# Optimization experiments

Measured on AMD Instinct MI355X. Metric: run time of the kernel, lower is better.

The kernel has to match this reference:

```python
import jax, jax.numpy as jnp
import numpy as np

N = 50000      # num nodes
IN = 256       # in_channels
H = 4          # heads
C = 64         # out_channels per head (concat=False -> out_dim = C)
HOPS = 3       # max_hops == num hops provided
E = 400000     # edges per hop
NEG_SLOPE = 0.2


def setup_inputs() -> dict:
    key = jax.random.key(0)
    ks = jax.random.split(key, 10)
    s_in = 1.0 / np.sqrt(IN)
    s_c = 1.0 / np.sqrt(C)
    return {
        "x": jax.random.normal(ks[0], (N, IN), jnp.float32),
        "ei0": jax.random.randint(ks[1], (2, E), 0, N, dtype=jnp.int32),
        "ei1": jax.random.randint(ks[2], (2, E), 0, N, dtype=jnp.int32),
        "ei2": jax.random.randint(ks[3], (2, E), 0, N, dtype=jnp.int32),
        # shared left/right projections (lin_l / lin_r, shared across hops)
        "W_l": jax.random.normal(ks[4], (IN, H * C), jnp.float32) * s_in,
        "b_l": jnp.zeros((H * C,), jnp.float32),
        "W_r": jax.random.normal(ks[5], (IN, H * C), jnp.float32) * s_in,
        "b_r": jnp.zeros((H * C,), jnp.float32),
        # hop-specific attention vectors and output biases
        "att": jax.random.normal(ks[6], (HOPS, H, C), jnp.float32) * s_c,
        "bias": jnp.zeros((HOPS, C), jnp.float32),
        # hop gate (single Linear since gate_hidden=None)
        "W_gate": jax.random.normal(ks[7], (IN, HOPS), jnp.float32) * s_in,
        "b_gate": jnp.zeros((HOPS,), jnp.float32),
    }


def _segment_softmax(logits, seg, n):
    # logits: [E, H], seg: [E] destination node ids
    m = jax.ops.segment_max(logits, seg, num_segments=n)          # [N, H]
    m = jnp.where(jnp.isfinite(m), m, 0.0)                        # empty segments -> 0
    ex = jnp.exp(logits - m[seg])
    s = jax.ops.segment_sum(ex, seg, num_segments=n)              # [N, H]
    return ex / (s[seg] + 1e-16)


def _gatv2_hop(x_l, x_r, edge_index, att_k, bias_k):
    # x_l, x_r: [N, H, C] shared projections; edge_index: [2, Ek]
    src, dst = edge_index[0], edge_index[1]
    s = jax.nn.leaky_relu(x_l[src] + x_r[dst], NEG_SLOPE)         # [Ek, H, C]
    alpha = jnp.einsum("ehc,hc->eh", s, att_k)                    # [Ek, H]
    alpha = _segment_softmax(alpha, dst, N)
    msg = jax.ops.segment_sum(x_l[src] * alpha[..., None], dst, num_segments=N)  # [N, H, C]
    return msg.mean(axis=1) + bias_k                              # concat=False -> head mean, [N, C]


def reference(x, ei0, ei1, ei2, W_l, b_l, W_r, b_r, att, bias, W_gate, b_gate):
    # shared projections computed once
    x_l = (x @ W_l + b_l).reshape(N, H, C)
    x_r = (x @ W_r + b_r).reshape(N, H, C)

    # hop 0 gets self-loops (add_self_loops=True); higher hops do not
    ar = jnp.arange(N, dtype=ei0.dtype)
    ei0_sl = jnp.concatenate([ei0, jnp.stack([ar, ar])], axis=1)
    edges = [ei0_sl, ei1, ei2]

    messages = jnp.stack(
        [_gatv2_hop(x_l, x_r, edges[k], att[k], bias[k]) for k in range(HOPS)],
        axis=1,
    )  # [N, HOPS, C]

    logits = x @ W_gate + b_gate                                  # [N, HOPS]
    weights = jax.nn.softmax(logits, axis=-1)
    out = jnp.einsum("nkc,nk->nc", messages, weights)             # [N, C]
    return out
```

## Files before the change

### kernel.cpp

```cpp
#include <hip/hip_runtime.h>
#include <math.h>

#define N_NODES 50000
#define IN_DIM 256
#define HEADS 4
#define CDIM 64
#define HC 256
#define HOPS 3
#define EDGES 400000
#define NEG_SLOPE 0.2f
#define SEG (EDGES + N_NODES)
#define TOT_E (3 * EDGES + N_NODES)
#define CAP 40

#define NB_GATE  ((N_NODES + 3) / 4)
#define NB_PACKW ((IN_DIM * 2 * HC) / 256)
#define NB_SCAT  ((TOT_E + 255) / 256)
#define GB 64
#define GEMM_BLOCKS ((N_NODES + GB - 1) / GB)
#define AP 264
#define BP 40

typedef unsigned short ushort;
using short8  = __attribute__((ext_vector_type(8))) short;
using floatx4 = __attribute__((ext_vector_type(4))) float;
using f32x2   = __attribute__((ext_vector_type(2))) float;

__device__ __forceinline__ void decode_flat(int f, int& k, int& e)
{
    if (f < SEG)              { k = 0; e = f; }
    else if (f < SEG + EDGES) { k = 1; e = f - SEG; }
    else                      { k = 2; e = f - SEG - EDGES; }
}

__device__ __forceinline__ ushort f2bf(float f)
{
    unsigned u = __float_as_uint(f);
    unsigned r = u + 0x7fffu + ((u >> 16) & 1u);
    return (ushort)(r >> 16);
}

__device__ __forceinline__ f32x2 bf2x(unsigned u)
{
    f32x2 r;
    r.x = __uint_as_float(u << 16);
    r.y = __uint_as_float(u & 0xffff0000u);
    return r;
}

__device__ __forceinline__ f32x2 lrelu2(f32x2 v)
{
    return __builtin_elementwise_max(v, 0.2f * v);
}

__global__ __launch_bounds__(256) void prep(
    const float* __restrict__ X, const float* __restrict__ Wg,
    const float* __restrict__ bg, float* __restrict__ gw,
    ushort* __restrict__ Xb,
    const float* __restrict__ Wl, const float* __restrict__ Wr,
    ushort* __restrict__ WT,
    const int* __restrict__ ei0, const int* __restrict__ ei1,
    const int* __restrict__ ei2, int* __restrict__ cnt,
    int* __restrict__ bucket)
{
    const int blk = blockIdx.x;
    const int tid = threadIdx.x;

    if (blk < NB_GATE) {
        const int node = (blk * 256 + tid) >> 6;
        const int lane = tid & 63;
        if (node >= N_NODES) return;

        float4 xv = ((const float4*)(X + (size_t)node * IN_DIM))[lane];

        union { ushort s[4]; uint2 u; } o;
        o.s[0] = f2bf(xv.x); o.s[1] = f2bf(xv.y);
        o.s[2] = f2bf(xv.z); o.s[3] = f2bf(xv.w);
        ((uint2*)(Xb + (size_t)node * IN_DIM))[lane] = o.u;

        float a0 = 0.f, a1 = 0.f, a2 = 0.f;
        const int i0 = lane * 4;
        a0 += xv.x * Wg[(i0 + 0) * HOPS + 0]; a1 += xv.x * Wg[(i0 + 0) * HOPS + 1]; a2 += xv.x * Wg[(i0 + 0) * HOPS + 2];
        a0 += xv.y * Wg[(i0 + 1) * HOPS + 0]; a1 += xv.y * Wg[(i0 + 1) * HOPS + 1]; a2 += xv.y * Wg[(i0 + 1) * HOPS + 2];
        a0 += xv.z * Wg[(i0 + 2) * HOPS + 0]; a1 += xv.z * Wg[(i0 + 2) * HOPS + 1]; a2 += xv.z * Wg[(i0 + 2) * HOPS + 2];
        a0 += xv.w * Wg[(i0 + 3) * HOPS + 0]; a1 += xv.w * Wg[(i0 + 3) * HOPS + 1]; a2 += xv.w * Wg[(i0 + 3) * HOPS + 2];

        #pragma unroll
        for (int off = 32; off >= 1; off >>= 1) {
            a0 += __shfl_xor(a0, off);
            a1 += __shfl_xor(a1, off);
            a2 += __shfl_xor(a2, off);
        }
        if (lane == 0) {
            float l0 = a0 + bg[0], l1 = a1 + bg[1], l2 = a2 + bg[2];
            float m = fmaxf(l0, fmaxf(l1, l2));
            float e0 = expf(l0 - m), e1 = expf(l1 - m), e2 = expf(l2 - m);
            float inv = 1.f / (e0 + e1 + e2);
            gw[node * HOPS + 0] = e0 * inv;
            gw[node * HOPS + 1] = e1 * inv;
            gw[node * HOPS + 2] = e2 * inv;
        }
    } else if (blk < NB_GATE + NB_PACKW) {
        int id = (blk - NB_GATE) * 256 + tid;
        int n = id >> 8;
        int k = id & 255;
        float v = (n < HC) ? Wl[k * HC + n] : Wr[k * HC + (n - HC)];
        WT[(size_t)n * IN_DIM + k] = f2bf(v);
    } else {
        int f = (blk - NB_GATE - NB_PACKW) * 256 + tid;
        if (f >= TOT_E) return;
        int k, e; decode_flat(f, k, e);
        int s, d;
        if (k == 0 && e >= EDGES) { s = d = e - EDGES; }
        else {
            const int* ei = (k == 0) ? ei0 : (k == 1) ? ei1 : ei2;
            s = ei[e]; d = ei[EDGES + e];
        }
        int pos = atomicAdd(&cnt[k * N_NODES + d], 1);
        if (pos < CAP)
            bucket[((size_t)k * N_NODES + d) * CAP + pos] = s;
    }
}

__global__ __launch_bounds__(256, 2) void gemm_mfma(
    const ushort* __restrict__ Xb, const ushort* __restrict__ WT,
    const float* __restrict__ b_l, const float* __restrict__ b_r,
    ushort* __restrict__ xlb, ushort* __restrict__ xrb, int M)
{
    __shared__ ushort As[GB][AP];
    __shared__ ushort Bs[512][BP];
    const int tid  = threadIdx.x;
    const int wave = tid >> 6, lane = tid & 63;
    const int row0 = blockIdx.x * GB;
    const int wx   = wave * 128;
    const int lrow = lane & 15, lk = (lane >> 4) * 8;

    #pragma unroll
    for (int j = 0; j < 8; j++) {
        int id = tid + 256 * j;
        int r  = id >> 5;
        int c  = (id & 31) * 8;
        int gr = row0 + r;
        uint4 v = make_uint4(0u, 0u, 0u, 0u);
        if (gr < M)
            v = *(const uint4*)(Xb + (size_t)gr * IN_DIM + c);
        *(uint4*)&As[r][c] = v;
    }

    floatx4 acc[4][8];
    #pragma unroll
    for (int i = 0; i < 4; i++)
        #pragma unroll
        for (int j = 0; j < 8; j++)
            acc[i][j] = (floatx4){0.f, 0.f, 0.f, 0.f};

    for (int k0 = 0; k0 < IN_DIM; k0 += 32) {
        __syncthreads();
        #pragma unroll
        for (int j = 0; j < 8; j++) {
            int id = tid + 256 * j;
            int r  = id >> 2;
            int c  = (id & 3) * 8;
            *(uint4*)&Bs[r][c] =
                *(const uint4*)(WT + (size_t)r * IN_DIM + k0 + c);
        }
        __syncthreads();

        short8 af[4], bf[8];
        #pragma unroll
        for (int mi = 0; mi < 4; mi++)
            af[mi] = *(const short8*)&As[mi * 16 + lrow][k0 + lk];
        #pragma unroll
        for (int ni = 0; ni < 8; ni++)
            bf[ni] = *(const short8*)&Bs[wx + ni * 16 + lrow][lk];

        #pragma unroll
        for (int mi = 0; mi < 4; mi++)
            #pragma unroll
            for (int ni = 0; ni < 8; ni++)
                acc[mi][ni] = __builtin_amdgcn_mfma_f32_16x16x32_bf16(
                    bf[ni], af[mi], acc[mi][ni], 0, 0, 0);
    }

    const int csub = (lane >> 4) * 4;
    const bool left = (wx < HC);
    const float*  bvec = left ? b_l : b_r;
    ushort*       obuf = left ? xlb : xrb;
    const int     cbase = left ? wx : wx - HC;
    #pragma unroll
    for (int mi = 0; mi < 4; mi++) {
        int grow = row0 + mi * 16 + lrow;
        if (grow < M) {
            #pragma unroll
            for (int ni = 0; ni < 8; ni++) {
                int lc = cbase + ni * 16 + csub;
                floatx4 v = acc[mi][ni];
                const float4 b = *(const float4*)(bvec + lc);
                union { ushort s[4]; uint2 u; } o;
                o.s[0] = f2bf(v[0] + b.x);
                o.s[1] = f2bf(v[1] + b.y);
                o.s[2] = f2bf(v[2] + b.z);
                o.s[3] = f2bf(v[3] + b.w);
                *(uint2*)(obuf + (size_t)grow * HC + lc) = o.u;
            }
        }
    }
}

__global__ __launch_bounds__(192) void node_all(
    const ushort* __restrict__ xlb, const ushort* __restrict__ xrb,
    const int* __restrict__ cnt, const int* __restrict__ bucket,
    const float* __restrict__ att, const float* __restrict__ gw,
    const float* __restrict__ bias, float* __restrict__ out)
{
    __shared__ float lds[HOPS][CDIM];
    const int n    = blockIdx.x;
    const int k    = threadIdx.x >> 6;
    const int lane = threadIdx.x & 63;
    const int half = lane >> 5;
    const int sub  = lane & 31;
    const unsigned laneoff = (unsigned)sub * 8;

    const int deg = min(cnt[k * N_NODES + n], CAP);
    const int* bk = bucket + ((size_t)k * N_NODES + n) * CAP;

    uint4 rq = *(const uint4*)(xrb + (size_t)n * HC + laneoff);
    f32x2 rr[4] = { bf2x(rq.x), bf2x(rq.y), bf2x(rq.z), bf2x(rq.w) };

    const float4 a0 = ((const float4*)(att + (size_t)k * HC))[sub * 2 + 0];
    const float4 a1 = ((const float4*)(att + (size_t)k * HC))[sub * 2 + 1];
    f32x2 w2[4] = { {a0.x, a0.y}, {a0.z, a0.w}, {a1.x, a1.y}, {a1.z, a1.w} };

    float denom = 0.f;
    f32x2 acc2[4] = { {0.f,0.f}, {0.f,0.f}, {0.f,0.f}, {0.f,0.f} };

    if (deg > 0) {
        const int degm1 = deg - 1;
        int myS = (lane < deg) ? bk[lane] : 0;
        const int npair = (deg + 1) >> 1;

        int s0 = __shfl(myS, min(half, degm1));
        uint4 q = *(const uint4*)(xlb + (unsigned)s0 * HC + laneoff);

        for (int j = 0; j < npair; j++) {
            int sn = __shfl(myS, min(2 * (j + 1) + half, degm1));
            uint4 qn = *(const uint4*)(xlb + (unsigned)sn * HC + laneoff);

            f32x2 f0 = bf2x(q.x), f1 = bf2x(q.y);
            f32x2 f2 = bf2x(q.z), f3 = bf2x(q.w);

            f32x2 pp = w2[0] * lrelu2(f0 + rr[0]);
            pp = __builtin_elementwise_fma(w2[1], lrelu2(f1 + rr[1]), pp);
            pp = __builtin_elementwise_fma(w2[2], lrelu2(f2 + rr[2]), pp);
            pp = __builtin_elementwise_fma(w2[3], lrelu2(f3 + rr[3]), pp);
            float p = pp.x + pp.y;

            p += __shfl_xor(p, 1);
            p += __shfl_xor(p, 2);
            p += __shfl_xor(p, 4);

            bool valid = (2 * j + half) < deg;
            float ex = valid ? __expf(p) : 0.f;
            denom += ex;
            f32x2 ex2 = { ex, ex };
            acc2[0] = __builtin_elementwise_fma(ex2, f0, acc2[0]);
            acc2[1] = __builtin_elementwise_fma(ex2, f1, acc2[1]);
            acc2[2] = __builtin_elementwise_fma(ex2, f2, acc2[2]);
            acc2[3] = __builtin_elementwise_fma(ex2, f3, acc2[3]);
            q = qn;
        }
    }

    denom += __shfl_xor(denom, 32);
    const float inv = (denom > 0.f) ? 1.f / denom : 0.f;
    const float g   = gw[n * HOPS + k];
    const float* bb = bias + (size_t)k * CDIM + (size_t)(sub & 7) * 8;

    #pragma unroll
    for (int i = 0; i < 4; i++) {
        acc2[i].x += __shfl_xor(acc2[i].x, 32);
        acc2[i].y += __shfl_xor(acc2[i].y, 32);
        acc2[i].x *= inv;
        acc2[i].y *= inv;
        acc2[i].x += __shfl_xor(acc2[i].x, 8);
        acc2[i].y += __shfl_xor(acc2[i].y, 8);
        acc2[i].x += __shfl_xor(acc2[i].x, 16);
        acc2[i].y += __shfl_xor(acc2[i].y, 16);
        if (lane < 8) {
            lds[k][lane * 8 + 2 * i]     = g * (acc2[i].x * 0.25f + bb[2 * i]);
            lds[k][lane * 8 + 2 * i + 1] = g * (acc2[i].y * 0.25f + bb[2 * i + 1]);
        }
    }
    __syncthreads();

    if (threadIdx.x < CDIM)
        out[(size_t)n * CDIM + threadIdx.x] =
            lds[0][threadIdx.x] + lds[1][threadIdx.x] + lds[2][threadIdx.x];
}

extern "C" void kernel_launch(void* const* d_in, const int* in_sizes, int n_in,
                              void* d_out, int out_size, void* d_ws, size_t ws_size,
                              hipStream_t stream)
{
    const float* x      = (const float*)d_in[0];
    const int*   ei0    = (const int*)d_in[1];
    const int*   ei1    = (const int*)d_in[2];
    const int*   ei2    = (const int*)d_in[3];
    const float* W_l    = (const float*)d_in[4];
    const float* b_l    = (const float*)d_in[5];
    const float* W_r    = (const float*)d_in[6];
    const float* b_r    = (const float*)d_in[7];
    const float* att    = (const float*)d_in[8];
    const float* bias   = (const float*)d_in[9];
    const float* W_gate = (const float*)d_in[10];
    const float* b_gate = (const float*)d_in[11];

    const size_t NHC = (size_t)N_NODES * HC;
    float* ws      = (float*)d_ws;
    float* gwbuf   = ws;
    int*   cnt     = (int*)(gwbuf + HOPS * N_NODES);
    int*   bucket  = cnt + HOPS * N_NODES;
    ushort* xlb    = (ushort*)(bucket + (size_t)HOPS * N_NODES * CAP);
    ushort* xrb    = xlb + NHC;
    ushort* Xb     = xrb + NHC;
    ushort* WT     = Xb + NHC;

    hipMemsetAsync(cnt, 0, (size_t)HOPS * N_NODES * sizeof(int), stream);

    prep<<<NB_GATE + NB_PACKW + NB_SCAT, 256, 0, stream>>>(
        x, W_gate, b_gate, gwbuf, Xb, W_l, W_r, WT,
        ei0, ei1, ei2, cnt, bucket);

    gemm_mfma<<<GEMM_BLOCKS, 256, 0, stream>>>(Xb, WT, b_l, b_r, xlb, xrb, N_NODES);

    node_all<<<N_NODES, 192, 0, stream>>>(
        xlb, xrb, cnt, bucket, att, gwbuf, bias, (float*)d_out);
}
```

Baseline: 387.7 us.

## Fuse edge scatter into GEMM launch, drop B staging, use raw exp2

Moves the count zeroing from a hipMemsetAsync into the prep kernel and moves the edge bucketing scatter into the GEMM launch as extra blocks, so the scatter can overlap the MFMA work. The GEMM no longer stages the weight tile in LDS: each wave reads its B fragments straight from global/L2, which removes two barriers per k-step at the cost of uncoalesced, repeated global reads. The attention softmax folds log2(e) into the attention vector and uses raw v_exp_f32 in place of __expf, which saves a multiply per edge.

After: 346.6 us. 10.6% less time.

```diff
diff --git a/kernel.cpp b/kernel.cpp
--- a/kernel.cpp
+++ b/kernel.cpp
@@ -12,14 +12,16 @@
 #define SEG (EDGES + N_NODES)
 #define TOT_E (3 * EDGES + N_NODES)
 #define CAP 40
+#define LOG2E 1.44269504f
 
 #define NB_GATE  ((N_NODES + 3) / 4)
 #define NB_PACKW ((IN_DIM * 2 * HC) / 256)
+#define NB_ZERO  ((HOPS * N_NODES + 255) / 256)
 #define NB_SCAT  ((TOT_E + 255) / 256)
 #define GB 64
-#define GEMM_BLOCKS ((N_NODES + GB - 1) / GB)
 #define AP 264
-#define BP 40
+#define GEMM_BLKS  ((N_NODES + GB - 1) / GB)
+#define FUSED_BLKS (GEMM_BLKS + NB_SCAT)
 
 typedef unsigned short ushort;
 using short8  = __attribute__((ext_vector_type(8))) short;
@@ -40,6 +42,13 @@
     return (ushort)(r >> 16);
 }
 
+__device__ __forceinline__ float exp2_raw(float x)
+{
+    float r;
+    asm volatile("v_exp_f32 %0, %1" : "=v"(r) : "v"(x));
+    return r;
+}
+
 __device__ __forceinline__ f32x2 bf2x(unsigned u)
 {
     f32x2 r;
@@ -53,15 +62,12 @@
     return __builtin_elementwise_max(v, 0.2f * v);
 }
 
-__global__ __launch_bounds__(256) void prep(
+__global__ __launch_bounds__(256) void prep_a(
     const float* __restrict__ X, const float* __restrict__ Wg,
     const float* __restrict__ bg, float* __restrict__ gw,
     ushort* __restrict__ Xb,
     const float* __restrict__ Wl, const float* __restrict__ Wr,
-    ushort* __restrict__ WT,
-    const int* __restrict__ ei0, const int* __restrict__ ei1,
-    const int* __restrict__ ei2, int* __restrict__ cnt,
-    int* __restrict__ bucket)
+    ushort* __restrict__ WT, int* __restrict__ cnt)
 {
     const int blk = blockIdx.x;
     const int tid = threadIdx.x;
@@ -107,7 +113,25 @@
         float v = (n < HC) ? Wl[k * HC + n] : Wr[k * HC + (n - HC)];
         WT[(size_t)n * IN_DIM + k] = f2bf(v);
     } else {
-        int f = (blk - NB_GATE - NB_PACKW) * 256 + tid;
+        int id = (blk - NB_GATE - NB_PACKW) * 256 + tid;
+        if (id < HOPS * N_NODES) cnt[id] = 0;
+    }
+}
+
+__global__ __launch_bounds__(256, 2) void gemm_scatter(
+    const ushort* __restrict__ Xb, const ushort* __restrict__ WT,
+    const float* __restrict__ b_l, const float* __restrict__ b_r,
+    ushort* __restrict__ xlb, ushort* __restrict__ xrb, int M,
+    const int* __restrict__ ei0, const int* __restrict__ ei1,
+    const int* __restrict__ ei2, int* __restrict__ cnt,
+    int* __restrict__ bucket)
+{
+    __shared__ ushort As[GB][AP];
+    const int blk = blockIdx.x;
+    const int tid = threadIdx.x;
+
+    if (blk >= GEMM_BLKS) {
+        int f = (blk - GEMM_BLKS) * 256 + tid;
         if (f >= TOT_E) return;
         int k, e; decode_flat(f, k, e);
         int s, d;
@@ -119,19 +143,11 @@
         int pos = atomicAdd(&cnt[k * N_NODES + d], 1);
         if (pos < CAP)
             bucket[((size_t)k * N_NODES + d) * CAP + pos] = s;
-    }
-}
-
-__global__ __launch_bounds__(256, 2) void gemm_mfma(
-    const ushort* __restrict__ Xb, const ushort* __restrict__ WT,
-    const float* __restrict__ b_l, const float* __restrict__ b_r,
-    ushort* __restrict__ xlb, ushort* __restrict__ xrb, int M)
-{
-    __shared__ ushort As[GB][AP];
-    __shared__ ushort Bs[512][BP];
-    const int tid  = threadIdx.x;
+        return;
+    }
+
     const int wave = tid >> 6, lane = tid & 63;
-    const int row0 = blockIdx.x * GB;
+    const int row0 = blk * GB;
     const int wx   = wave * 128;
     const int lrow = lane & 15, lk = (lane >> 4) * 8;
 
@@ -146,6 +162,7 @@
             v = *(const uint4*)(Xb + (size_t)gr * IN_DIM + c);
         *(uint4*)&As[r][c] = v;
     }
+    __syncthreads();
 
     floatx4 acc[4][8];
     #pragma unroll
@@ -154,25 +171,16 @@
         for (int j = 0; j < 8; j++)
             acc[i][j] = (floatx4){0.f, 0.f, 0.f, 0.f};
 
+    #pragma unroll 2
     for (int k0 = 0; k0 < IN_DIM; k0 += 32) {
-        __syncthreads();
-        #pragma unroll
-        for (int j = 0; j < 8; j++) {
-            int id = tid + 256 * j;
-            int r  = id >> 2;
-            int c  = (id & 3) * 8;
-            *(uint4*)&Bs[r][c] =
-                *(const uint4*)(WT + (size_t)r * IN_DIM + k0 + c);
-        }
-        __syncthreads();
-
         short8 af[4], bf[8];
+        #pragma unroll
+        for (int ni = 0; ni < 8; ni++)
+            bf[ni] = *(const short8*)(WT +
+                (size_t)(wx + ni * 16 + lrow) * IN_DIM + k0 + lk);
         #pragma unroll
         for (int mi = 0; mi < 4; mi++)
             af[mi] = *(const short8*)&As[mi * 16 + lrow][k0 + lk];
-        #pragma unroll
-        for (int ni = 0; ni < 8; ni++)
-            bf[ni] = *(const short8*)&Bs[wx + ni * 16 + lrow][lk];
 
         #pragma unroll
         for (int mi = 0; mi < 4; mi++)
@@ -229,7 +237,8 @@
 
     const float4 a0 = ((const float4*)(att + (size_t)k * HC))[sub * 2 + 0];
     const float4 a1 = ((const float4*)(att + (size_t)k * HC))[sub * 2 + 1];
-    f32x2 w2[4] = { {a0.x, a0.y}, {a0.z, a0.w}, {a1.x, a1.y}, {a1.z, a1.w} };
+    f32x2 w2[4] = { {a0.x * LOG2E, a0.y * LOG2E}, {a0.z * LOG2E, a0.w * LOG2E},
+                    {a1.x * LOG2E, a1.y * LOG2E}, {a1.z * LOG2E, a1.w * LOG2E} };
 
     float denom = 0.f;
     f32x2 acc2[4] = { {0.f,0.f}, {0.f,0.f}, {0.f,0.f}, {0.f,0.f} };
@@ -260,7 +269,7 @@
             p += __shfl_xor(p, 4);
 
             bool valid = (2 * j + half) < deg;
-            float ex = valid ? __expf(p) : 0.f;
+            float ex = valid ? exp2_raw(p) : 0.f;
             denom += ex;
             f32x2 ex2 = { ex, ex };
             acc2[0] = __builtin_elementwise_fma(ex2, f0, acc2[0]);
@@ -325,13 +334,12 @@
     ushort* Xb     = xrb + NHC;
     ushort* WT     = Xb + NHC;
 
-    hipMemsetAsync(cnt, 0, (size_t)HOPS * N_NODES * sizeof(int), stream);
-
-    prep<<<NB_GATE + NB_PACKW + NB_SCAT, 256, 0, stream>>>(
-        x, W_gate, b_gate, gwbuf, Xb, W_l, W_r, WT,
+    prep_a<<<NB_GATE + NB_PACKW + NB_ZERO, 256, 0, stream>>>(
+        x, W_gate, b_gate, gwbuf, Xb, W_l, W_r, WT, cnt);
+
+    gemm_scatter<<<FUSED_BLKS, 256, 0, stream>>>(
+        Xb, WT, b_l, b_r, xlb, xrb, N_NODES,
         ei0, ei1, ei2, cnt, bucket);
-
-    gemm_mfma<<<GEMM_BLOCKS, 256, 0, stream>>>(Xb, WT, b_l, b_r, xlb, xrb, N_NODES);
 
     node_all<<<N_NODES, 192, 0, stream>>>(
         xlb, xrb, cnt, bucket, att, gwbuf, bias, (float*)d_out);
```
